# Kernel optimization log

Measured on AMD Instinct MI355X. Metric: run time of the kernel, lower is better.

Reference implementation:

```python
import jax, jax.numpy as jnp
import numpy as np

B, S, D, H = 2, 2048, 1024, 16
HD = D // H
SCALING = HD ** -0.5


def _length_mask(lengths, seqlen):
    return (jnp.arange(seqlen)[None, :] < jnp.asarray(lengths)[:, None]).astype(jnp.int32)


def setup_inputs() -> dict:
    key = jax.random.key(0)
    ks = jax.random.split(key, 10)
    std = D ** -0.5
    inp = {
        "hidden_states": jax.random.normal(ks[0], (B, S, D), dtype=jnp.float32),
        "Wq": jax.random.normal(ks[1], (D, D), dtype=jnp.float32) * std,
        "bq": jax.random.normal(ks[2], (D,), dtype=jnp.float32) * 0.02,
        "Wk": jax.random.normal(ks[3], (D, D), dtype=jnp.float32) * std,
        "bk": jax.random.normal(ks[4], (D,), dtype=jnp.float32) * 0.02,
        "Wv": jax.random.normal(ks[5], (D, D), dtype=jnp.float32) * std,
        "bv": jax.random.normal(ks[6], (D,), dtype=jnp.float32) * 0.02,
        "Wo": jax.random.normal(ks[7], (D, D), dtype=jnp.float32) * std,
        "bo": jax.random.normal(ks[8], (D,), dtype=jnp.float32) * 0.02,
        # variable valid lengths per batch element (padding at the end)
        "query_mask_1d": _length_mask([S, S - 512], S),
        "key_mask_1d": _length_mask([S, S - 512], S),
    }
    return inp


def reference(hidden_states, Wq, bq, Wk, bk, Wv, bv, Wo, bo, query_mask_1d, key_mask_1d):
    bsz, tgt_len, _ = hidden_states.shape
    # projections (dropout p=0 / eval -> identity)
    q = (hidden_states @ Wq + bq) * SCALING
    k = hidden_states @ Wk + bk
    v = hidden_states @ Wv + bv
    q = q.reshape(bsz, tgt_len, H, HD).transpose(0, 2, 1, 3)  # [B,H,S,HD]
    k = k.reshape(bsz, -1, H, HD).transpose(0, 2, 1, 3)
    v = v.reshape(bsz, -1, H, HD).transpose(0, 2, 1, 3)

    scores = jnp.einsum("bhqd,bhkd->bhqk", q, k)  # [B,H,S,S]
    q_valid = (query_mask_1d != 0)[:, None, :, None]  # [B,1,S,1]
    k_valid = (key_mask_1d != 0)[:, None, None, :]    # [B,1,1,S]
    # masked_fill(-inf) on padded keys; padded-query rows would be all -inf ->
    # softmax NaN -> nan_to_num(0). We compute the same result NaN-free by
    # zeroing the scores of padded-query rows and zeroing their probs after.
    s = jnp.where(k_valid, scores, -jnp.inf)
    s = jnp.where(q_valid, s, 0.0)
    attn_weights = jax.nn.softmax(s, axis=-1) * q_valid  # == softmax + nan_to_num

    attn_output = jnp.einsum("bhqk,bhkd->bhqd", attn_weights, v)
    attn_output = attn_output.transpose(0, 2, 1, 3).reshape(bsz, tgt_len, D)
    attn_output = attn_output @ Wo + bo
    return attn_output
```

## Files before the change

### kernel.cpp

```cpp
#include <hip/hip_runtime.h>
#include <stdint.h>

#define BB 2
#define SS 2048
#define DD 1024
#define HH 16
#define HDIM 64
#define MTOT (BB*SS)
#define QK_SCALE_LOG2E 0.180336880f

typedef unsigned short u16;
typedef __attribute__((ext_vector_type(8))) __bf16 bf16x8;
typedef __attribute__((ext_vector_type(4))) float f32x4;

static __device__ __forceinline__ float exp2_hw(float x) {
    return __builtin_amdgcn_exp2f(x);
}

static __device__ __forceinline__ u16 f2bu(float f) {
    union { float f; uint32_t u; } c; c.f = f;
    uint32_t u = c.u + 0x7fffu + ((c.u >> 16) & 1u);
    return (u16)(u >> 16);
}

static __device__ __forceinline__ u16 f2b_hw(float f) {
    __bf16 b = (__bf16)f;
    union { __bf16 b; u16 u; } c; c.b = b;
    return c.u;
}

static __device__ __forceinline__ uint32_t cvt_pk_bf16(float lo, float hi) {
    uint32_t r;
    asm("v_cvt_pk_bf16_f32 %0, %1, %2" : "=v"(r) : "v"(lo), "v"(hi));
    return r;
}

static __device__ __forceinline__ void gload_lds16(const void* g, void* l) {
    __builtin_amdgcn_global_load_lds(
        (const __attribute__((address_space(1))) uint32_t*)(g),
        (__attribute__((address_space(3))) uint32_t*)(l),
        16, 0, 0);
}

__global__ void k_prep(const float* __restrict__ x, u16* __restrict__ xb,
                       const float* __restrict__ Wq, const float* __restrict__ Wk,
                       const float* __restrict__ Wv, const float* __restrict__ Wo,
                       u16* __restrict__ Wqkv_t, u16* __restrict__ Wo_t) {
    const int which = blockIdx.z;
    if (which == 4) {
        const int tid = (blockIdx.y * 32 + blockIdx.x) * 256 + threadIdx.y * 32 + threadIdx.x;
        #pragma unroll
        for (int r = 0; r < 4; ++r) {
            const int i = (tid + r * 262144) * 4;
            float4 v = *(const float4*)(x + i);
            ushort4 o;
            o.x = f2bu(v.x); o.y = f2bu(v.y); o.z = f2bu(v.z); o.w = f2bu(v.w);
            *(ushort4*)(xb + i) = o;
        }
        return;
    }
    __shared__ float tile[32][33];
    const float* W = (which == 0) ? Wq : (which == 1) ? Wk : (which == 2) ? Wv : Wo;
    u16* dst = (which < 3) ? (Wqkv_t + (size_t)which * DD * DD) : Wo_t;
    const int n0 = blockIdx.x * 32, k0 = blockIdx.y * 32;
    const int tx = threadIdx.x, ty = threadIdx.y;
    #pragma unroll
    for (int i = 0; i < 32; i += 8)
        tile[ty + i][tx] = W[(size_t)(k0 + ty + i) * DD + (n0 + tx)];
    __syncthreads();
    #pragma unroll
    for (int i = 0; i < 32; i += 8)
        dst[(size_t)(n0 + ty + i) * DD + (k0 + tx)] = f2bu(tile[tx][ty + i]);
}

#define VMH(N) do { asm volatile("s_waitcnt vmcnt(" #N ")" ::: "memory"); \
                    __builtin_amdgcn_sched_barrier(0); } while (0)

#define PHX(AFRC, BFRC, MFQ, RDNEXT, STAGECODE)                               \
  { RDNEXT;                                                                   \
    STAGECODE;                                                                \
    __builtin_amdgcn_s_barrier();                                             \
    __builtin_amdgcn_sched_barrier(0);                                        \
    __builtin_amdgcn_s_setprio(1);                                            \
    _Pragma("unroll") for (int m2 = 0; m2 < 2; ++m2)                          \
      _Pragma("unroll") for (int nf = 0; nf < 3; ++nf)                        \
        _Pragma("unroll") for (int ks = 0; ks < 2; ++ks)                      \
          acc[2*(MFQ)+m2][nf] = __builtin_amdgcn_mfma_f32_16x16x32_bf16(      \
              AFRC[m2][ks], BFRC[nf][ks], acc[2*(MFQ)+m2][nf], 0, 0, 0);      \
    __builtin_amdgcn_s_setprio(0);                                            \
    __builtin_amdgcn_s_barrier();                                             \
  }

__global__ __launch_bounds__(512, 2) void k_gemm_qkv(
    const u16* __restrict__ Xb, const u16* __restrict__ Wt,
    const float* __restrict__ bq, const float* __restrict__ bk_, const float* __restrict__ bv,
    u16* __restrict__ Qb, u16* __restrict__ Kb, u16* __restrict__ Vt)
{
    __shared__ u16 AsA[3][256 * 64];
    __shared__ u16 BsB[2][192 * 64];

    const int flat = blockIdx.y * 16 + blockIdx.x;
    const int xcd = flat & 7, idx = flat >> 3;
    const int by = ((xcd >> 1) << 2) + (idx >> 3);
    const int bx = ((xcd & 1) << 3) + (idx & 7);
    const int m0 = by << 8, n0 = bx * 192;

    const int t = threadIdx.x;
    const int lane = t & 63, w = t >> 6;
    const int wm = (w >> 2) << 7, wn = (w & 3) * 48;
    const int lr = lane & 15, lg = lane >> 4;

    const u16* Asrc = Xb + (size_t)m0 * DD;
    const u16* Bsrc = Wt + (size_t)n0 * DD;

    f32x4 acc[8][3] = {};
    bf16x8 afr0[2][2], afr1[2][2];
    bf16x8 bfr0[3][2], bfr1[3][2];

    auto stgA = [&](u16* bufp, int half, int tt) {
        #pragma unroll
        for (int r = 0; r < 2; ++r) {
            int off = (t + (r << 9)) << 4;
            int row = off >> 7, colb = off & 127;
            int scol = colb ^ ((row & 7) << 4);
            gload_lds16(Asrc + (size_t)((half << 7) + row) * DD + (tt << 6) + (scol >> 1),
                        (char*)bufp + (half << 14) + off);
        }
    };
    auto stgB = [&](u16* bufp, int tt) {
        #pragma unroll
        for (int r = 0; r < 3; ++r) {
            int off = (t + (r << 9)) << 4;
            int row = off >> 7, colb = off & 127;
            int scol = colb ^ ((row & 7) << 4);
            gload_lds16(Bsrc + (size_t)row * DD + (tt << 6) + (scol >> 1),
                        (char*)bufp + off);
        }
    };

    auto rdA = [&](const u16* bufp, int mf, int ks) {
        const int row = wm + (mf << 4) + lr;
        const int col = ((ks << 6) + (lg << 4)) ^ ((row & 7) << 4);
        return *(const bf16x8*)((const char*)bufp + row * 128 + col);
    };
    auto rdB = [&](const u16* bufp, int nf, int ks) {
        const int row = wn + (nf << 4) + lr;
        const int col = ((ks << 6) + (lg << 4)) ^ ((row & 7) << 4);
        return *(const bf16x8*)((const char*)bufp + row * 128 + col);
    };
    auto rdAq = [&](bf16x8 (&dst)[2][2], const u16* bufp, int q) {
        #pragma unroll
        for (int m2 = 0; m2 < 2; ++m2)
            #pragma unroll
            for (int ks = 0; ks < 2; ++ks)
                dst[m2][ks] = rdA(bufp, 2 * q + m2, ks);
    };
    auto rdBt = [&](bf16x8 (&dst)[3][2], const u16* bufp) {
        #pragma unroll
        for (int nf = 0; nf < 3; ++nf)
            #pragma unroll
            for (int ks = 0; ks < 2; ++ks)
                dst[nf][ks] = rdB(bufp, nf, ks);
    };

    u16* pE = AsA[0]; u16* pO = AsA[1]; u16* pS = AsA[2];
    u16* Bs0 = BsB[0]; u16* Bs1 = BsB[1];

    stgA(pE, 0, 0); stgA(pE, 1, 0); stgB(Bs0, 0);
    stgA(pO, 0, 1); stgA(pO, 1, 1); stgB(Bs1, 1);
    asm volatile("s_waitcnt vmcnt(7)" ::: "memory");
    __builtin_amdgcn_sched_barrier(0);
    __builtin_amdgcn_s_barrier();
    rdAq(afr0, pE, 0);
    rdBt(bfr0, Bs0);

    #pragma unroll 1
    for (int j = 0; j < 7; ++j) {
        const int tb = 2 * j;
        PHX(afr0, bfr0, 0, { rdAq(afr1, pE, 1); }, { stgA(pS, 0, tb + 2); });
        PHX(afr1, bfr0, 1, { rdAq(afr0, pE, 2); }, { stgA(pS, 1, tb + 2); });
        PHX(afr0, bfr0, 2, { rdAq(afr1, pE, 3); }, { stgB(Bs0, tb + 2); });
        VMH(7);
        PHX(afr1, bfr0, 3, { rdAq(afr0, pO, 0); rdBt(bfr1, Bs1); }, {});
        PHX(afr0, bfr1, 0, { rdAq(afr1, pO, 1); }, { stgA(pE, 0, tb + 3); });
        PHX(afr1, bfr1, 1, { rdAq(afr0, pO, 2); }, { stgA(pE, 1, tb + 3); });
        PHX(afr0, bfr1, 2, { rdAq(afr1, pO, 3); }, { stgB(Bs1, tb + 3); });
        VMH(7);
        PHX(afr1, bfr1, 3, { rdAq(afr0, pS, 0); rdBt(bfr0, Bs0); }, {});
        u16* oE = pE; u16* oO = pO; u16* oS = pS;
        pE = oS; pO = oE; pS = oO;
    }
    PHX(afr0, bfr0, 0, { rdAq(afr1, pE, 1); }, {});
    PHX(afr1, bfr0, 1, { rdAq(afr0, pE, 2); }, {});
    PHX(afr0, bfr0, 2, { rdAq(afr1, pE, 3); }, {});
    VMH(0);
    PHX(afr1, bfr0, 3, { rdAq(afr0, pO, 0); rdBt(bfr1, Bs1); }, {});
    PHX(afr0, bfr1, 0, { rdAq(afr1, pO, 1); }, {});
    PHX(afr1, bfr1, 1, { rdAq(afr0, pO, 2); }, {});
    PHX(afr0, bfr1, 2, { rdAq(afr1, pO, 3); }, {});
    PHX(afr1, bfr1, 3, {}, {});

    #pragma unroll
    for (int mf = 0; mf < 8; ++mf) {
        #pragma unroll
        for (int nf = 0; nf < 3; ++nf) {
            const int n = n0 + wn + (nf << 4) + lr;
            const int mbase = m0 + wm + (mf << 4) + (lg << 2);
            const int b_ = mbase >> 11;
            const int s_ = mbase & 2047;
            const int seg = n >> 10;
            const int nn = n & 1023;
            const int hh = nn >> 6, d = nn & 63;
            if (seg == 0) {
                const float bias = bq[nn];
                u16* dstp = Qb + (((size_t)b_ * HH + hh) * SS + s_) * HDIM + d;
                #pragma unroll
                for (int r = 0; r < 4; ++r)
                    dstp[(size_t)r * HDIM] = f2bu((acc[mf][nf][r] + bias) * QK_SCALE_LOG2E);
            } else if (seg == 1) {
                const float bias = bk_[nn];
                u16* dstp = Kb + (((size_t)b_ * HH + hh) * SS + s_) * HDIM + d;
                #pragma unroll
                for (int r = 0; r < 4; ++r)
                    dstp[(size_t)r * HDIM] = f2bu(acc[mf][nf][r] + bias);
            } else {
                const float bias = bv[nn];
                ushort4 pk;
                pk.x = f2bu(acc[mf][nf][0] + bias);
                pk.y = f2bu(acc[mf][nf][1] + bias);
                pk.z = f2bu(acc[mf][nf][2] + bias);
                pk.w = f2bu(acc[mf][nf][3] + bias);
                *(ushort4*)(Vt + (((size_t)b_ * HH + hh) * HDIM + d) * SS + s_) = pk;
            }
        }
    }
}

__global__ __launch_bounds__(512, 4) void k_attn(
    const u16* __restrict__ Qb, const u16* __restrict__ Kb, const u16* __restrict__ Vt,
    const int* __restrict__ qmask, const int* __restrict__ kmask,
    u16* __restrict__ X2)
{
    const int i = blockIdx.x;
    const int xcd = i & 7, j = i >> 3;
    const int qt = j & 15;
    const int bh = xcd + ((j >> 4) << 3);
    const int b_ = bh >> 4;
    const int h = bh & 15;

    const int t = threadIdx.x;
    const int lane = t & 63, w = t >> 6;
    const int lr = lane & 15, lg = lane >> 4;

    __shared__ u16 Ks[3][64 * 64];
    __shared__ u16 Vs[3][64 * 64];

    const int q0 = qt << 7;
    const size_t bhs = (size_t)b_ * HH + h;
    const u16* Qbase = Qb + bhs * SS * HDIM;
    const char* KbaseB = (const char*)(Kb + bhs * SS * HDIM);
    const char* VbaseB = (const char*)(Vt + bhs * HDIM * SS);

    if (qmask[b_ * SS + q0] == 0) {
        #pragma unroll
        for (int r = 0; r < 4; ++r) {
            const int q = q0 + (w << 4) + (lg << 2) + r;
            #pragma unroll
            for (int nf = 0; nf < 4; ++nf)
                X2[((size_t)b_ * SS + q) * DD + (h << 6) + (nf << 4) + lr] = 0;
        }
        return;
    }

    int kv = (lane < 32) ? kmask[b_ * SS + (lane << 6)] : 0;
    unsigned long long bal = __ballot(kv != 0);
    const int nkt = __popcll(bal);

    bf16x8 qf[2];
    #pragma unroll
    for (int ks = 0; ks < 2; ++ks)
        qf[ks] = *(const bf16x8*)(Qbase + (size_t)(q0 + (w << 4) + lr) * HDIM + (ks << 5) + (lg << 3));

    bf16x8 vones;
    #pragma unroll
    for (int i2 = 0; i2 < 8; ++i2) vones[i2] = (__bf16)1.0f;

    f32x4 o[4] = {};
    f32x4 lacc = {};

    auto stage = [&](int buf, int kb) {
        const int off = t << 4;
        const int row = off >> 7, colb = off & 127;
        const int scol = colb ^ ((row & 7) << 4);
        gload_lds16(KbaseB + (size_t)(kb + row) * 128 + scol, (char*)Ks[buf] + off);
        gload_lds16(VbaseB + ((size_t)row * SS + (size_t)kb) * 2 + scol, (char*)Vs[buf] + off);
    };

    if (nkt > 0) stage(0, 0);
    if (nkt > 1) stage(1, 64);
    if (nkt > 1) { asm volatile("s_waitcnt vmcnt(2)" ::: "memory"); }
    else         { asm volatile("s_waitcnt vmcnt(0)" ::: "memory"); }
    __builtin_amdgcn_sched_barrier(0);
    __builtin_amdgcn_s_barrier();

    int cur = 0;
    #pragma unroll 1
    for (int kt = 0; kt < nkt; ++kt) {
        const int kb = kt << 6;
        const int nxt = (cur == 2) ? 0 : cur + 1;
        const int nx2 = (nxt == 2) ? 0 : nxt + 1;
        if (kt + 2 < nkt) stage(nx2, kb + 128);

        f32x4 sf[4] = {};
        __builtin_amdgcn_s_setprio(1);
        #pragma unroll
        for (int ks = 0; ks < 2; ++ks) {
            #pragma unroll
            for (int f = 0; f < 4; ++f) {
                const int krow = (f << 4) + lr;
                const int kcol = ((ks << 6) + (lg << 4)) ^ ((krow & 7) << 4);
                bf16x8 kf = *(const bf16x8*)((const char*)Ks[cur] + krow * 128 + kcol);
                sf[f] = __builtin_amdgcn_mfma_f32_16x16x32_bf16(kf, qf[ks], sf[f], 0, 0, 0);
            }
        }
        __builtin_amdgcn_s_setprio(0);
        if (kt == nkt - 1) {
            #pragma unroll
            for (int f = 0; f < 4; ++f) {
                #pragma unroll
                for (int r = 0; r < 4; ++r) {
                    if (kmask[b_ * SS + kb + (f << 4) + (lg << 2) + r] == 0)
                        sf[f][r] = -1e30f;
                }
            }
        }
        #pragma unroll
        for (int f = 0; f < 4; ++f)
            #pragma unroll
            for (int r = 0; r < 4; ++r)
                sf[f][r] = exp2_hw(sf[f][r]);

        uint32_t wv[4][2];
        #pragma unroll
        for (int f = 0; f < 4; ++f) {
            wv[f][0] = cvt_pk_bf16(sf[f][0], sf[f][1]);
            wv[f][1] = cvt_pk_bf16(sf[f][2], sf[f][3]);
        }
        bf16x8 pa[2];
        #pragma unroll
        for (int ks2 = 0; ks2 < 2; ++ks2) {
            uint32_t u0, u1, u2, u3;
            {
                uint32_t A = wv[2 * ks2][0], B = wv[2 * ks2 + 1][0];
                asm("v_permlane32_swap_b32 %0, %1" : "+v"(A), "+v"(B));
                asm("v_permlane16_swap_b32 %0, %1" : "+v"(A), "+v"(B));
                u0 = A; u2 = B;
            }
            {
                uint32_t A = wv[2 * ks2][1], B = wv[2 * ks2 + 1][1];
                asm("v_permlane32_swap_b32 %0, %1" : "+v"(A), "+v"(B));
                asm("v_permlane16_swap_b32 %0, %1" : "+v"(A), "+v"(B));
                u1 = A; u3 = B;
            }
            union { uint32_t q[4]; bf16x8 v; } cv;
            cv.q[0] = u0; cv.q[1] = u1; cv.q[2] = u2; cv.q[3] = u3;
            pa[ks2] = cv.v;
        }

        __builtin_amdgcn_s_setprio(1);
        #pragma unroll
        for (int ks = 0; ks < 2; ++ks) {
            lacc = __builtin_amdgcn_mfma_f32_16x16x32_bf16(pa[ks], vones, lacc, 0, 0, 0);
            #pragma unroll
            for (int nf = 0; nf < 4; ++nf) {
                const int vrow = (nf << 4) + lr;
                const int vcol = ((ks << 6) + (lg << 4)) ^ ((vrow & 7) << 4);
                bf16x8 vb = *(const bf16x8*)((const char*)Vs[cur] + vrow * 128 + vcol);
                o[nf] = __builtin_amdgcn_mfma_f32_16x16x32_bf16(pa[ks], vb, o[nf], 0, 0, 0);
            }
        }
        __builtin_amdgcn_s_setprio(0);

        if (kt + 2 < nkt) { asm volatile("s_waitcnt vmcnt(2)" ::: "memory"); }
        else              { asm volatile("s_waitcnt vmcnt(0)" ::: "memory"); }
        __builtin_amdgcn_sched_barrier(0);
        __builtin_amdgcn_s_barrier();
        cur = nxt;
    }

    #pragma unroll
    for (int r = 0; r < 4; ++r) {
        const int q = q0 + (w << 4) + (lg << 2) + r;
        float l = lacc[r];
        float inv = (l > 0.f) ? __builtin_amdgcn_rcpf(l) : 0.f;
        if (qmask[b_ * SS + q] == 0) inv = 0.f;
        #pragma unroll
        for (int nf = 0; nf < 4; ++nf)
            X2[((size_t)b_ * SS + q) * DD + (h << 6) + (nf << 4) + lr] = f2b_hw(o[nf][r] * inv);
    }
}

__global__ __launch_bounds__(256, 2) void k_gemm_out(
    const u16* __restrict__ X2, const u16* __restrict__ Wot,
    const float* __restrict__ bo, float* __restrict__ out)
{
    __shared__ u16 As3[3][128 * 64];
    __shared__ u16 Bs3[3][128 * 64];
    const int flat = blockIdx.y * 8 + blockIdx.x;
    const int xcd = flat & 7, idx = flat >> 3;
    const int by = (xcd << 2) + (idx >> 3);
    const int bx = idx & 7;
    const int m0 = by * 128, n0 = bx * 128;
    const int t = threadIdx.x;
    const int lane = t & 63, w = t >> 6;
    const int wm = (w >> 1) << 6, wn = (w & 1) << 6;
    const int lr = lane & 15, lg = lane >> 4;

    f32x4 acc[4][4] = {};

    auto stage = [&](int buf, int kt) {
        #pragma unroll
        for (int i = 0; i < 4; ++i) {
            int off = (t + (i << 8)) << 4;
            int row = off >> 7, colb = off & 127;
            int scol = colb ^ ((row & 7) << 4);
            gload_lds16(X2 + (size_t)(m0 + row) * DD + (kt << 6) + (scol >> 1), (char*)As3[buf] + off);
            gload_lds16(Wot + (size_t)(n0 + row) * DD + (kt << 6) + (scol >> 1), (char*)Bs3[buf] + off);
        }
    };

    stage(0, 0); stage(1, 1);
    asm volatile("s_waitcnt vmcnt(8)" ::: "memory");
    __builtin_amdgcn_sched_barrier(0);
    __builtin_amdgcn_s_barrier();

    int cur = 0;
    #pragma unroll 1
    for (int kt = 0; kt < 16; ++kt) {
        const int nxt = (cur == 2) ? 0 : cur + 1;
        const int nx2 = (nxt == 2) ? 0 : nxt + 1;
        if (kt + 2 < 16) stage(nx2, kt + 2);

        __builtin_amdgcn_s_setprio(1);
        #pragma unroll
        for (int ks = 0; ks < 2; ++ks) {
            bf16x8 a[4], b[4];
            #pragma unroll
            for (int i = 0; i < 4; ++i) {
                const int row = wm + (i << 4) + lr;
                a[i] = *(const bf16x8*)((const char*)As3[cur] + row * 128 + (((ks << 6) + (lg << 4)) ^ ((row & 7) << 4)));
            }
            #pragma unroll
            for (int i = 0; i < 4; ++i) {
                const int row = wn + (i << 4) + lr;
                b[i] = *(const bf16x8*)((const char*)Bs3[cur] + row * 128 + (((ks << 6) + (lg << 4)) ^ ((row & 7) << 4)));
            }
            #pragma unroll
            for (int mi = 0; mi < 4; ++mi)
                #pragma unroll
                for (int ni = 0; ni < 4; ++ni)
                    acc[mi][ni] = __builtin_amdgcn_mfma_f32_16x16x32_bf16(a[mi], b[ni], acc[mi][ni], 0, 0, 0);
        }
        __builtin_amdgcn_s_setprio(0);

        if (kt < 15) {
            if (kt + 2 < 16) { asm volatile("s_waitcnt vmcnt(8)" ::: "memory"); }
            else             { asm volatile("s_waitcnt vmcnt(0)" ::: "memory"); }
            __builtin_amdgcn_sched_barrier(0);
            __builtin_amdgcn_s_barrier();
        }
        cur = nxt;
    }

    #pragma unroll
    for (int mi = 0; mi < 4; ++mi) {
        #pragma unroll
        for (int ni = 0; ni < 4; ++ni) {
            const int n = n0 + wn + (ni << 4) + lr;
            const int mbase = m0 + wm + (mi << 4) + (lg << 2);
            const float bias = bo[n];
            #pragma unroll
            for (int r = 0; r < 4; ++r)
                out[(size_t)(mbase + r) * DD + n] = acc[mi][ni][r] + bias;
        }
    }
}

extern "C" void kernel_launch(void* const* d_in, const int* in_sizes, int n_in,
                              void* d_out, int out_size, void* d_ws, size_t ws_size,
                              hipStream_t stream) {
    const float* hs = (const float*)d_in[0];
    const float* Wq = (const float*)d_in[1];
    const float* bq = (const float*)d_in[2];
    const float* Wk = (const float*)d_in[3];
    const float* bk = (const float*)d_in[4];
    const float* Wv = (const float*)d_in[5];
    const float* bv = (const float*)d_in[6];
    const float* Wo = (const float*)d_in[7];
    const float* bo = (const float*)d_in[8];
    const int* qm = (const int*)d_in[9];
    const int* km = (const int*)d_in[10];
    float* out = (float*)d_out;

    char* ws = (char*)d_ws;
    const size_t MB = 1024 * 1024;
    u16* Xb  = (u16*)(ws + 0);
    u16* Wt3 = (u16*)(ws + 8 * MB);
    u16* Wot = (u16*)(ws + 14 * MB);
    u16* Qb  = (u16*)(ws + 16 * MB);
    u16* Kb  = (u16*)(ws + 24 * MB);
    u16* Vt  = (u16*)(ws + 32 * MB);
    u16* X2  = (u16*)(ws + 40 * MB);

    k_prep<<<dim3(32, 32, 5), dim3(32, 8), 0, stream>>>(hs, Xb, Wq, Wk, Wv, Wo, Wt3, Wot);
    k_gemm_qkv<<<dim3(16, 16), dim3(512), 0, stream>>>(Xb, Wt3, bq, bk, bv, Qb, Kb, Vt);
    k_attn<<<dim3(512), dim3(512), 0, stream>>>(Qb, Kb, Vt, qm, km, X2);
    k_gemm_out<<<dim3(8, 32), dim3(256), 0, stream>>>(X2, Wot, bo, out);
}
```

Measured before the change: 104.8 us.

## Replace QKV GEMM 256x192 phased pipeline with simpler 128x128 triple-buffered tiles

The QKV projection GEMM drops its hand-scheduled 256x192 tile, 8-wave phased MFMA pipeline and uses 128x128 tiles with 4 waves per block. A simple triple-buffered LDS ring stages A and B together each k-step, with one barrier per iteration. The grid grows from 256 to 768 blocks. The aim is more blocks to spread over CUs and simpler synchronisation, at the cost of lower arithmetic intensity per block and less overlap of LDS reads with MFMA.

After: 133.3 us. 1.27x slower.

```diff
diff --git a/kernel.cpp b/kernel.cpp
--- a/kernel.cpp
+++ b/kernel.cpp
@@ -73,142 +73,88 @@
         dst[(size_t)(n0 + ty + i) * DD + (k0 + tx)] = f2bu(tile[tx][ty + i]);
 }
 
-#define VMH(N) do { asm volatile("s_waitcnt vmcnt(" #N ")" ::: "memory"); \
-                    __builtin_amdgcn_sched_barrier(0); } while (0)
-
-#define PHX(AFRC, BFRC, MFQ, RDNEXT, STAGECODE)                               \
-  { RDNEXT;                                                                   \
-    STAGECODE;                                                                \
-    __builtin_amdgcn_s_barrier();                                             \
-    __builtin_amdgcn_sched_barrier(0);                                        \
-    __builtin_amdgcn_s_setprio(1);                                            \
-    _Pragma("unroll") for (int m2 = 0; m2 < 2; ++m2)                          \
-      _Pragma("unroll") for (int nf = 0; nf < 3; ++nf)                        \
-        _Pragma("unroll") for (int ks = 0; ks < 2; ++ks)                      \
-          acc[2*(MFQ)+m2][nf] = __builtin_amdgcn_mfma_f32_16x16x32_bf16(      \
-              AFRC[m2][ks], BFRC[nf][ks], acc[2*(MFQ)+m2][nf], 0, 0, 0);      \
-    __builtin_amdgcn_s_setprio(0);                                            \
-    __builtin_amdgcn_s_barrier();                                             \
-  }
-
-__global__ __launch_bounds__(512, 2) void k_gemm_qkv(
+__global__ __launch_bounds__(256, 2) void k_gemm_qkv(
     const u16* __restrict__ Xb, const u16* __restrict__ Wt,
     const float* __restrict__ bq, const float* __restrict__ bk_, const float* __restrict__ bv,
     u16* __restrict__ Qb, u16* __restrict__ Kb, u16* __restrict__ Vt)
 {
-    __shared__ u16 AsA[3][256 * 64];
-    __shared__ u16 BsB[2][192 * 64];
-
-    const int flat = blockIdx.y * 16 + blockIdx.x;
+    __shared__ u16 As3[3][128 * 64];
+    __shared__ u16 Bs3[3][128 * 64];
+    const int flat = blockIdx.y * 24 + blockIdx.x;
     const int xcd = flat & 7, idx = flat >> 3;
-    const int by = ((xcd >> 1) << 2) + (idx >> 3);
-    const int bx = ((xcd & 1) << 3) + (idx & 7);
-    const int m0 = by << 8, n0 = bx * 192;
-
+    const int by = ((xcd >> 1) << 3) + idx / 12;
+    const int bx = ((xcd & 1) * 12) + idx % 12;
+    const int m0 = by << 7, n0 = bx << 7;
     const int t = threadIdx.x;
     const int lane = t & 63, w = t >> 6;
-    const int wm = (w >> 2) << 7, wn = (w & 3) * 48;
+    const int wm = (w >> 1) << 6, wn = (w & 1) << 6;
     const int lr = lane & 15, lg = lane >> 4;
 
-    const u16* Asrc = Xb + (size_t)m0 * DD;
-    const u16* Bsrc = Wt + (size_t)n0 * DD;
-
-    f32x4 acc[8][3] = {};
-    bf16x8 afr0[2][2], afr1[2][2];
-    bf16x8 bfr0[3][2], bfr1[3][2];
-
-    auto stgA = [&](u16* bufp, int half, int tt) {
-        #pragma unroll
-        for (int r = 0; r < 2; ++r) {
-            int off = (t + (r << 9)) << 4;
+    f32x4 acc[4][4] = {};
+
+    auto stage = [&](int buf, int kt) {
+        #pragma unroll
+        for (int i = 0; i < 4; ++i) {
+            int off = (t + (i << 8)) << 4;
             int row = off >> 7, colb = off & 127;
             int scol = colb ^ ((row & 7) << 4);
-            gload_lds16(Asrc + (size_t)((half << 7) + row) * DD + (tt << 6) + (scol >> 1),
-                        (char*)bufp + (half << 14) + off);
+            gload_lds16(Xb + (size_t)(m0 + row) * DD + (kt << 6) + (scol >> 1), (char*)As3[buf] + off);
+            gload_lds16(Wt + (size_t)(n0 + row) * DD + (kt << 6) + (scol >> 1), (char*)Bs3[buf] + off);
         }
     };
-    auto stgB = [&](u16* bufp, int tt) {
-        #pragma unroll
-        for (int r = 0; r < 3; ++r) {
-            int off = (t + (r << 9)) << 4;
-            int row = off >> 7, colb = off & 127;
-            int scol = colb ^ ((row & 7) << 4);
-            gload_lds16(Bsrc + (size_t)row * DD + (tt << 6) + (scol >> 1),
-                        (char*)bufp + off);
-        }
-    };
-
-    auto rdA = [&](const u16* bufp, int mf, int ks) {
-        const int row = wm + (mf << 4) + lr;
-        const int col = ((ks << 6) + (lg << 4)) ^ ((row & 7) << 4);
-        return *(const bf16x8*)((const char*)bufp + row * 128 + col);
-    };
-    auto rdB = [&](const u16* bufp, int nf, int ks) {
-        const int row = wn + (nf << 4) + lr;
-        const int col = ((ks << 6) + (lg << 4)) ^ ((row & 7) << 4);
-        return *(const bf16x8*)((const char*)bufp + row * 128 + col);
-    };
-    auto rdAq = [&](bf16x8 (&dst)[2][2], const u16* bufp, int q) {
-        #pragma unroll
-        for (int m2 = 0; m2 < 2; ++m2)
-            #pragma unroll
-            for (int ks = 0; ks < 2; ++ks)
-                dst[m2][ks] = rdA(bufp, 2 * q + m2, ks);
-    };
-    auto rdBt = [&](bf16x8 (&dst)[3][2], const u16* bufp) {
-        #pragma unroll
-        for (int nf = 0; nf < 3; ++nf)
-            #pragma unroll
-            for (int ks = 0; ks < 2; ++ks)
-                dst[nf][ks] = rdB(bufp, nf, ks);
-    };
-
-    u16* pE = AsA[0]; u16* pO = AsA[1]; u16* pS = AsA[2];
-    u16* Bs0 = BsB[0]; u16* Bs1 = BsB[1];
-
-    stgA(pE, 0, 0); stgA(pE, 1, 0); stgB(Bs0, 0);
-    stgA(pO, 0, 1); stgA(pO, 1, 1); stgB(Bs1, 1);
-    asm volatile("s_waitcnt vmcnt(7)" ::: "memory");
+
+    stage(0, 0); stage(1, 1);
+    asm volatile("s_waitcnt vmcnt(8)" ::: "memory");
     __builtin_amdgcn_sched_barrier(0);
     __builtin_amdgcn_s_barrier();
-    rdAq(afr0, pE, 0);
-    rdBt(bfr0, Bs0);
-
+
+    int cur = 0;
     #pragma unroll 1
-    for (int j = 0; j < 7; ++j) {
-        const int tb = 2 * j;
-        PHX(afr0, bfr0, 0, { rdAq(afr1, pE, 1); }, { stgA(pS, 0, tb + 2); });
-        PHX(afr1, bfr0, 1, { rdAq(afr0, pE, 2); }, { stgA(pS, 1, tb + 2); });
-        PHX(afr0, bfr0, 2, { rdAq(afr1, pE, 3); }, { stgB(Bs0, tb + 2); });
-        VMH(7);
-        PHX(afr1, bfr0, 3, { rdAq(afr0, pO, 0); rdBt(bfr1, Bs1); }, {});
-        PHX(afr0, bfr1, 0, { rdAq(afr1, pO, 1); }, { stgA(pE, 0, tb + 3); });
-        PHX(afr1, bfr1, 1, { rdAq(afr0, pO, 2); }, { stgA(pE, 1, tb + 3); });
-        PHX(afr0, bfr1, 2, { rdAq(afr1, pO, 3); }, { stgB(Bs1, tb + 3); });
-        VMH(7);
-        PHX(afr1, bfr1, 3, { rdAq(afr0, pS, 0); rdBt(bfr0, Bs0); }, {});
-        u16* oE = pE; u16* oO = pO; u16* oS = pS;
-        pE = oS; pO = oE; pS = oO;
-    }
-    PHX(afr0, bfr0, 0, { rdAq(afr1, pE, 1); }, {});
-    PHX(afr1, bfr0, 1, { rdAq(afr0, pE, 2); }, {});
-    PHX(afr0, bfr0, 2, { rdAq(afr1, pE, 3); }, {});
-    VMH(0);
-    PHX(afr1, bfr0, 3, { rdAq(afr0, pO, 0); rdBt(bfr1, Bs1); }, {});
-    PHX(afr0, bfr1, 0, { rdAq(afr1, pO, 1); }, {});
-    PHX(afr1, bfr1, 1, { rdAq(afr0, pO, 2); }, {});
-    PHX(afr0, bfr1, 2, { rdAq(afr1, pO, 3); }, {});
-    PHX(afr1, bfr1, 3, {}, {});
-
-    #pragma unroll
-    for (int mf = 0; mf < 8; ++mf) {
-        #pragma unroll
-        for (int nf = 0; nf < 3; ++nf) {
-            const int n = n0 + wn + (nf << 4) + lr;
-            const int mbase = m0 + wm + (mf << 4) + (lg << 2);
+    for (int kt = 0; kt < 16; ++kt) {
+        const int nxt = (cur == 2) ? 0 : cur + 1;
+        const int nx2 = (nxt == 2) ? 0 : nxt + 1;
+        if (kt + 2 < 16) stage(nx2, kt + 2);
+
+        __builtin_amdgcn_s_setprio(1);
+        #pragma unroll
+        for (int ks = 0; ks < 2; ++ks) {
+            bf16x8 a[4], b[4];
+            #pragma unroll
+            for (int i = 0; i < 4; ++i) {
+                const int row = wm + (i << 4) + lr;
+                a[i] = *(const bf16x8*)((const char*)As3[cur] + row * 128 + (((ks << 6) + (lg << 4)) ^ ((row & 7) << 4)));
+            }
+            #pragma unroll
+            for (int i = 0; i < 4; ++i) {
+                const int row = wn + (i << 4) + lr;
+                b[i] = *(const bf16x8*)((const char*)Bs3[cur] + row * 128 + (((ks << 6) + (lg << 4)) ^ ((row & 7) << 4)));
+            }
+            #pragma unroll
+            for (int mi = 0; mi < 4; ++mi)
+                #pragma unroll
+                for (int ni = 0; ni < 4; ++ni)
+                    acc[mi][ni] = __builtin_amdgcn_mfma_f32_16x16x32_bf16(a[mi], b[ni], acc[mi][ni], 0, 0, 0);
+        }
+        __builtin_amdgcn_s_setprio(0);
+
+        if (kt < 15) {
+            if (kt + 2 < 16) { asm volatile("s_waitcnt vmcnt(8)" ::: "memory"); }
+            else             { asm volatile("s_waitcnt vmcnt(0)" ::: "memory"); }
+            __builtin_amdgcn_sched_barrier(0);
+            __builtin_amdgcn_s_barrier();
+        }
+        cur = nxt;
+    }
+
+    const int seg = bx >> 3;
+    #pragma unroll
+    for (int mi = 0; mi < 4; ++mi) {
+        #pragma unroll
+        for (int ni = 0; ni < 4; ++ni) {
+            const int n = n0 + wn + (ni << 4) + lr;
+            const int mbase = m0 + wm + (mi << 4) + (lg << 2);
             const int b_ = mbase >> 11;
             const int s_ = mbase & 2047;
-            const int seg = n >> 10;
             const int nn = n & 1023;
             const int hh = nn >> 6, d = nn & 63;
             if (seg == 0) {
@@ -216,20 +162,20 @@
                 u16* dstp = Qb + (((size_t)b_ * HH + hh) * SS + s_) * HDIM + d;
                 #pragma unroll
                 for (int r = 0; r < 4; ++r)
-                    dstp[(size_t)r * HDIM] = f2bu((acc[mf][nf][r] + bias) * QK_SCALE_LOG2E);
+                    dstp[(size_t)r * HDIM] = f2bu((acc[mi][ni][r] + bias) * QK_SCALE_LOG2E);
             } else if (seg == 1) {
                 const float bias = bk_[nn];
                 u16* dstp = Kb + (((size_t)b_ * HH + hh) * SS + s_) * HDIM + d;
                 #pragma unroll
                 for (int r = 0; r < 4; ++r)
-                    dstp[(size_t)r * HDIM] = f2bu(acc[mf][nf][r] + bias);
+                    dstp[(size_t)r * HDIM] = f2bu(acc[mi][ni][r] + bias);
             } else {
                 const float bias = bv[nn];
                 ushort4 pk;
-                pk.x = f2bu(acc[mf][nf][0] + bias);
-                pk.y = f2bu(acc[mf][nf][1] + bias);
-                pk.z = f2bu(acc[mf][nf][2] + bias);
-                pk.w = f2bu(acc[mf][nf][3] + bias);
+                pk.x = f2bu(acc[mi][ni][0] + bias);
+                pk.y = f2bu(acc[mi][ni][1] + bias);
+                pk.z = f2bu(acc[mi][ni][2] + bias);
+                pk.w = f2bu(acc[mi][ni][3] + bias);
                 *(ushort4*)(Vt + (((size_t)b_ * HH + hh) * HDIM + d) * SS + s_) = pk;
             }
         }
@@ -513,7 +459,7 @@
     u16* X2  = (u16*)(ws + 40 * MB);
 
     k_prep<<<dim3(32, 32, 5), dim3(32, 8), 0, stream>>>(hs, Xb, Wq, Wk, Wv, Wo, Wt3, Wot);
-    k_gemm_qkv<<<dim3(16, 16), dim3(512), 0, stream>>>(Xb, Wt3, bq, bk, bv, Qb, Kb, Vt);
+    k_gemm_qkv<<<dim3(24, 32), dim3(256), 0, stream>>>(Xb, Wt3, bq, bk, bv, Qb, Kb, Vt);
     k_attn<<<dim3(512), dim3(512), 0, stream>>>(Qb, Kb, Vt, qm, km, X2);
     k_gemm_out<<<dim3(8, 32), dim3(256), 0, stream>>>(X2, Wot, bo, out);
 }
```
